# Kernel tuning notes

Hardware: AMD Instinct MI355X
Metric: run time of the kernel (lower is better)

The kernel has to match this reference:

```python
import jax, jax.numpy as jnp
import numpy as np

D = 256          # d_model
NH = 8           # n_heads
HD = D // NH
LEV = 3          # n_levels
NP = 4           # n_points
DFF = 1024       # d_ffn
B = 8            # batch
LQ = 3600        # 60*60 queries (hardcoded in get_reference_points)
SHAPES = np.array([[60, 60], [30, 30], [15, 15]], dtype=np.int64)
LIN = int((SHAPES[:, 0] * SHAPES[:, 1]).sum())  # 4725
START = np.concatenate([[0], np.cumsum(SHAPES[:, 0] * SHAPES[:, 1])[:-1]]).astype(np.int64)


def setup_inputs() -> dict:
    key = jax.random.key(0)
    ks = iter(jax.random.split(key, 32))
    def lin(k, o, i):
        return jax.random.normal(k, (o, i), jnp.float32) * 0.02
    return {
        "tgt": jax.random.normal(next(ks), (LQ, B, D), jnp.float32),
        "query_pos": jax.random.normal(next(ks), (1, 1, D), jnp.float32),
        "src": jax.random.normal(next(ks), (B, LIN, D), jnp.float32),
        "src_spatial_shapes": jnp.asarray(SHAPES),
        "level_start_index": jnp.asarray(START),
        "in_proj_w": lin(next(ks), 3 * D, D),
        "in_proj_b": jnp.zeros((3 * D,), jnp.float32),
        "out_proj_w": lin(next(ks), D, D),
        "out_proj_b": jnp.zeros((D,), jnp.float32),
        "samp_off_w": lin(next(ks), NH * LEV * NP * 2, D),
        "samp_off_b": jax.random.normal(next(ks), (NH * LEV * NP * 2,), jnp.float32) * 0.5,
        "attn_w_w": lin(next(ks), NH * LEV * NP, D),
        "attn_w_b": jnp.zeros((NH * LEV * NP,), jnp.float32),
        "value_proj_w": lin(next(ks), D, D),
        "value_proj_b": jnp.zeros((D,), jnp.float32),
        "cross_out_w": lin(next(ks), D, D),
        "cross_out_b": jnp.zeros((D,), jnp.float32),
        "ln1_g": jnp.ones((D,), jnp.float32), "ln1_b": jnp.zeros((D,), jnp.float32),
        "ln2_g": jnp.ones((D,), jnp.float32), "ln2_b": jnp.zeros((D,), jnp.float32),
        "ln3_g": jnp.ones((D,), jnp.float32), "ln3_b": jnp.zeros((D,), jnp.float32),
        "ffn_w1": lin(next(ks), DFF, D), "ffn_b1": jnp.zeros((DFF,), jnp.float32),
        "ffn_w2": lin(next(ks), D, DFF), "ffn_b2": jnp.zeros((D,), jnp.float32),
    }


def _ln(x, g, b, eps=1e-5):
    m = x.mean(-1, keepdims=True)
    v = ((x - m) ** 2).mean(-1, keepdims=True)
    return (x - m) * jax.lax.rsqrt(v + eps) * g + b


def _self_attn(q_in, k_in, v_in, wqkv, bqkv, wo, bo):
    # torch nn.MultiheadAttention semantics, inputs laid out (seq, batch, embed)
    S, N, _ = q_in.shape
    q = (q_in @ wqkv[:D].T + bqkv[:D]).reshape(S, N, NH, HD)
    k = (k_in @ wqkv[D:2 * D].T + bqkv[D:2 * D]).reshape(S, N, NH, HD)
    v = (v_in @ wqkv[2 * D:].T + bqkv[2 * D:]).reshape(S, N, NH, HD)
    logits = jnp.einsum('snhd,tnhd->nhst', q, k) / np.sqrt(HD).astype(np.float32)
    a = jax.nn.softmax(logits, -1)
    ctx = jnp.einsum('nhst,tnhd->snhd', a, v).reshape(S, N, D)
    return ctx @ wo.T + bo


def _bilinear(v_l, loc, Hl, Wl):
    # v_l: [B, NH, Hl*Wl, HD]; loc: [B, NH, LQ, NP, 2] normalized in [0,1]
    # grid_sample(align_corners=False, padding=zeros): pixel = loc*size - 0.5
    x = loc[..., 0] * Wl - 0.5
    y = loc[..., 1] * Hl - 0.5
    x0 = jnp.floor(x); y0 = jnp.floor(y)
    fx = x - x0; fy = y - y0
    x0 = x0.astype(jnp.int32); y0 = y0.astype(jnp.int32)
    def corner(yi, xi, w):
        valid = ((xi >= 0) & (xi < Wl) & (yi >= 0) & (yi < Hl)).astype(v_l.dtype)
        idx = jnp.clip(yi, 0, Hl - 1) * Wl + jnp.clip(xi, 0, Wl - 1)
        b, h, lq, p = idx.shape
        g = jnp.take_along_axis(v_l, idx.reshape(b, h, lq * p)[..., None], axis=2)
        return g.reshape(b, h, lq, p, HD) * (w * valid)[..., None]
    return (corner(y0, x0, (1 - fx) * (1 - fy))
            + corner(y0, x0 + 1, fx * (1 - fy))
            + corner(y0 + 1, x0, (1 - fx) * fy)
            + corner(y0 + 1, x0 + 1, fx * fy))


def _msdeform(query, ref, src, wso, bso, waw, baw, wv, bv, wo, bo):
    Bq, Lq, _ = query.shape
    value = (src @ wv.T + bv).reshape(Bq, LIN, NH, HD).transpose(0, 2, 1, 3)  # [B,NH,LIN,HD]
    off = (query @ wso.T + bso).reshape(Bq, Lq, NH, LEV, NP, 2)
    aw = (query @ waw.T + baw).reshape(Bq, Lq, NH, LEV * NP)
    aw = jax.nn.softmax(aw, -1).reshape(Bq, Lq, NH, LEV, NP)
    normalizer = jnp.asarray(SHAPES[:, ::-1].copy(), jnp.float32)  # (W, H) per level
    loc = ref[:, :, None, :, None, :] + off / normalizer[None, None, None, :, None, :]
    out = jnp.zeros((Bq, NH, Lq, HD), query.dtype)
    for l in range(LEV):
        Hl, Wl = int(SHAPES[l, 0]), int(SHAPES[l, 1])
        s = int(START[l])
        v_l = value[:, :, s:s + Hl * Wl]
        loc_l = loc[:, :, :, l].transpose(0, 2, 1, 3, 4)      # [B,NH,LQ,NP,2]
        sampled = _bilinear(v_l, loc_l, Hl, Wl)               # [B,NH,LQ,NP,HD]
        out = out + (sampled * aw[:, :, :, l].transpose(0, 2, 1, 3)[..., None]).sum(3)
    out = out.transpose(0, 2, 1, 3).reshape(Bq, Lq, D)
    return out @ wo.T + bo


def _reference_points():
    Hh = Ww = 60
    ys = (jnp.arange(Hh, dtype=jnp.float32) + 0.5) / Hh
    xs = (jnp.arange(Ww, dtype=jnp.float32) + 0.5) / Ww
    yy, xx = jnp.meshgrid(ys, xs, indexing='ij')
    ref = jnp.stack([xx.reshape(-1), yy.reshape(-1)], -1)[None]  # [1, 3600, 2]
    return jnp.broadcast_to(ref[:, :, None, :], (1, Hh * Ww, LEV, 2))


def reference(tgt, query_pos, src, src_spatial_shapes, level_start_index,
              in_proj_w, in_proj_b, out_proj_w, out_proj_b,
              samp_off_w, samp_off_b, attn_w_w, attn_w_b,
              value_proj_w, value_proj_b, cross_out_w, cross_out_b,
              ln1_g, ln1_b, ln2_g, ln2_b, ln3_g, ln3_b,
              ffn_w1, ffn_b1, ffn_w2, ffn_b2):
    # dropout layers are identity (eval mode). spatial shapes are static metadata
    # (SHAPES/START) since slicing sizes must be static under jit.
    q = (tgt + query_pos).transpose(1, 0, 2)
    tgt2 = _self_attn(q, q, tgt.transpose(1, 0, 2), in_proj_w, in_proj_b, out_proj_w, out_proj_b)
    t = _ln(tgt + tgt2.transpose(1, 0, 2), ln2_g, ln2_b)
    ref = _reference_points()
    tq = t.transpose(1, 0, 2)  # permute(1,0,2) -> [B, LQ, D]
    tgt2 = _msdeform(tq + query_pos, ref, src, samp_off_w, samp_off_b,
                     attn_w_w, attn_w_b, value_proj_w, value_proj_b,
                     cross_out_w, cross_out_b)
    tq = _ln(tq + tgt2, ln1_g, ln1_b)
    ff = jax.nn.relu(tq @ ffn_w1.T + ffn_b1) @ ffn_w2.T + ffn_b2
    tq = _ln(tq + ff, ln3_g, ln3_b)
    return tq.transpose(1, 0, 2)  # [LQ, B, D]
```

## Files before the change

### kernel.cpp

```cpp
#include <hip/hip_runtime.h>
#include <hip/hip_bf16.h>
#include <cstddef>
#include <cstdint>

#define D_MODEL 256
#define NHEAD   8
#define HDIM    32
#define NLEV    3
#define NPNT    4
#define DFF     1024
#define BATCH   8
#define LQ      3600
#define LIN     4725
#define MROWS   (BATCH*LQ)

typedef short bf16x8 __attribute__((ext_vector_type(8)));
typedef float f32x4  __attribute__((ext_vector_type(4)));

__device__ __forceinline__ unsigned short f2b(float x) {
    unsigned int u = __float_as_uint(x);
    unsigned int r = (u + 0x7fffu + ((u >> 16) & 1u)) >> 16;
    return (unsigned short)r;
}
__device__ __forceinline__ float b2f(unsigned short s) {
    return __uint_as_float(((unsigned int)s) << 16);
}

#define GLDS16(g, l) __builtin_amdgcn_global_load_lds( \
    (const __attribute__((address_space(1))) void*)(g), \
    (__attribute__((address_space(3))) void*)(l), 16, 0, 0)

#define WAIT_VM0()  asm volatile("s_waitcnt vmcnt(0)" ::: "memory")
#define WAIT_LGKM0() asm volatile("s_waitcnt lgkmcnt(0)" ::: "memory")

#define WTOT 991232
__global__ __launch_bounds__(256) void prep_kernel(
    const float* __restrict__ tgt, unsigned short* __restrict__ tgtb,
    const float* __restrict__ srcf, unsigned short* __restrict__ srcb,
    const float* __restrict__ w_in, const float* __restrict__ w_out,
    const float* __restrict__ w_val, const float* __restrict__ w_cross,
    const float* __restrict__ w_so, const float* __restrict__ w_aw,
    const float* __restrict__ w_f1, const float* __restrict__ w_f2,
    unsigned short* __restrict__ wdst,
    const float* __restrict__ qp, const float* __restrict__ so_b,
    const float* __restrict__ aw_b, float* __restrict__ qpv)
{
    const int bid = blockIdx.x;
    const int tid = threadIdx.x;
    if (bid < 7200) {
        int i = bid * 256 + tid;
        float4 v = ((const float4*)tgt)[i];
        ushort4 o; o.x = f2b(v.x); o.y = f2b(v.y); o.z = f2b(v.z); o.w = f2b(v.w);
        ((ushort4*)tgtb)[i] = o;
    } else if (bid < 16650) {
        int i = (bid - 7200) * 256 + tid;
        float4 v = ((const float4*)srcf)[i];
        ushort4 o; o.x = f2b(v.x); o.y = f2b(v.y); o.z = f2b(v.z); o.w = f2b(v.w);
        ((ushort4*)srcb)[i] = o;
    } else if (bid < 17618) {
        int idx = ((bid - 16650) * 256 + tid) * 4;
        if (idx >= WTOT) return;
        const float* src; int off;
        if      (idx < 196608) { src = w_in;    off = idx; }
        else if (idx < 262144) { src = w_out;   off = idx - 196608; }
        else if (idx < 327680) { src = w_val;   off = idx - 262144; }
        else if (idx < 393216) { src = w_cross; off = idx - 327680; }
        else if (idx < 442368) { src = w_so;    off = idx - 393216; }
        else if (idx < 466944) { src = w_aw;    off = idx - 442368; }
        else if (idx < 729088) { src = w_f1;    off = idx - 466944; }
        else                   { src = w_f2;    off = idx - 729088; }
        float4 v = *(const float4*)(src + off);
        ushort4 o; o.x = f2b(v.x); o.y = f2b(v.y); o.z = f2b(v.z); o.w = f2b(v.w);
        *(ushort4*)(wdst + idx) = o;
    } else {
        int o = (bid - 17618) * 256 + tid;
        if (o >= 768 + 192 + 96) return;
        const float* wrow;
        if (o < 768)       wrow = w_in + (size_t)o * D_MODEL;
        else if (o < 960)  wrow = w_so + (size_t)(o - 768) * D_MODEL;
        else               wrow = w_aw + (size_t)(o - 960) * D_MODEL;
        float acc = 0.f;
        for (int d = 0; d < D_MODEL; ++d) acc += qp[d] * wrow[d];
        qpv[o] = acc;
        if (o >= 768) {
            float bias = (o < 960) ? so_b[o - 768] : aw_b[o - 960];
            qpv[1056 + (o - 768)] = acc + bias;
        }
    }
}

__global__ __launch_bounds__(256) void gemm_bf16(
    const unsigned short* __restrict__ A,
    const unsigned short* __restrict__ W,
    const float* __restrict__ bias,
    const float* __restrict__ bias2, int b2lim,
    float* __restrict__ Cf, unsigned short* __restrict__ Cb,
    int M, int N, int K, int relu)
{
    __shared__ __align__(16) unsigned short As[2 * 128 * 32];
    __shared__ __align__(16) unsigned short Bs[2 * 128 * 32];
    const int tid  = threadIdx.x;
    const int wave = tid >> 6;
    const int lane = tid & 63;
    const int m0 = blockIdx.x * 128;
    const int n0 = blockIdx.y * 128;

    const int lr  = lane >> 2;
    const int lc8 = (lane & 3) * 8;
    int ar0 = m0 + wave * 32 + lr;      if (ar0 > M - 1) ar0 = M - 1;
    int ar1 = m0 + wave * 32 + 16 + lr; if (ar1 > M - 1) ar1 = M - 1;
    int br0 = n0 + wave * 32 + lr;      if (br0 > N - 1) br0 = N - 1;
    int br1 = n0 + wave * 32 + 16 + lr; if (br1 > N - 1) br1 = N - 1;
    const unsigned short* pa0 = A + (size_t)ar0 * K + lc8;
    const unsigned short* pa1 = A + (size_t)ar1 * K + lc8;
    const unsigned short* pb0 = W + (size_t)br0 * K + lc8;
    const unsigned short* pb1 = W + (size_t)br1 * K + lc8;
    unsigned short* la0 = As + wave * 1024;
    unsigned short* la1 = As + wave * 1024 + 512;
    unsigned short* lb0 = Bs + wave * 1024;
    unsigned short* lb1 = Bs + wave * 1024 + 512;

    const int wm = (wave >> 1) * 64;
    const int wn = (wave & 1) * 64;
    const int fr = lane & 15;
    const int fk = (lane >> 4) * 8;

    f32x4 acc[4][4] = {};

    for (int k0 = 0; k0 < K; k0 += 64) {
        GLDS16(pa0, la0); GLDS16(pa0 + 32, la0 + 4096);
        GLDS16(pa1, la1); GLDS16(pa1 + 32, la1 + 4096);
        GLDS16(pb0, lb0); GLDS16(pb0 + 32, lb0 + 4096);
        GLDS16(pb1, lb1); GLDS16(pb1 + 32, lb1 + 4096);
        pa0 += 64; pa1 += 64; pb0 += 64; pb1 += 64;
        __syncthreads();
#pragma unroll
        for (int p = 0; p < 2; ++p) {
            bf16x8 af[4], bfv[4];
#pragma unroll
            for (int i = 0; i < 4; ++i)
                af[i] = *(const bf16x8*)&As[p * 4096 + (wm + i * 16 + fr) * 32 + fk];
#pragma unroll
            for (int j = 0; j < 4; ++j)
                bfv[j] = *(const bf16x8*)&Bs[p * 4096 + (wn + j * 16 + fr) * 32 + fk];
#pragma unroll
            for (int i = 0; i < 4; ++i)
#pragma unroll
                for (int j = 0; j < 4; ++j)
                    acc[i][j] = __builtin_amdgcn_mfma_f32_16x16x32_bf16(
                        af[i], bfv[j], acc[i][j], 0, 0, 0);
        }
        __syncthreads();
    }

    const int quad = lane >> 4;
#pragma unroll
    for (int j = 0; j < 4; ++j) {
        const int col = n0 + wn + j * 16 + fr;
        if (col >= N) continue;
        float bv = 0.f;
        if (bias) bv += bias[col];
        if (bias2 && col < b2lim) bv += bias2[col];
#pragma unroll
        for (int i = 0; i < 4; ++i) {
#pragma unroll
            for (int r = 0; r < 4; ++r) {
                const int row = m0 + wm + i * 16 + quad * 4 + r;
                if (row >= M) continue;
                float v = acc[i][j][r] + bv;
                if (relu) v = fmaxf(v, 0.f);
                if (Cf) Cf[(size_t)row * N + col] = v;
                if (Cb) Cb[(size_t)row * N + col] = f2b(v);
            }
        }
    }
}

__global__ __launch_bounds__(256) void gemm_ln(
    const unsigned short* __restrict__ A,
    const unsigned short* __restrict__ W,
    const float* __restrict__ bias,
    const float* __restrict__ resid,
    const float* __restrict__ g, const float* __restrict__ bb,
    float* __restrict__ outf, unsigned short* __restrict__ outb, int K)
{
    __shared__ __align__(16) unsigned short As[2 * 64 * 32];
    __shared__ __align__(16) unsigned short Bs[2 * 256 * 32];
    const int tid  = threadIdx.x;
    const int wave = tid >> 6;
    const int lane = tid & 63;
    const int m0 = blockIdx.x * 64;

    const int arow = tid >> 2;
    const int akc  = (tid & 3) * 8;
    const unsigned short* pa = A + (size_t)(m0 + arow) * K + akc;
    unsigned short* la = As + tid * 8;
    const unsigned short* pb0 = W + (size_t)(arow)       * K + akc;
    const unsigned short* pb1 = W + (size_t)(64  + arow) * K + akc;
    const unsigned short* pb2 = W + (size_t)(128 + arow) * K + akc;
    const unsigned short* pb3 = W + (size_t)(192 + arow) * K + akc;
    unsigned short* lb0 = Bs + tid * 8;
    unsigned short* lb1 = Bs + 2048 + tid * 8;
    unsigned short* lb2 = Bs + 4096 + tid * 8;
    unsigned short* lb3 = Bs + 6144 + tid * 8;

    const int fr = lane & 15;
    const int fk = (lane >> 4) * 8;
    const int quad = lane >> 4;
    const int colbase = wave * 64;

    f32x4 acc[4][4] = {};

    for (int k0 = 0; k0 < K; k0 += 64) {
        GLDS16(pa, la);        GLDS16(pa + 32, la + 2048);
        GLDS16(pb0, lb0);      GLDS16(pb0 + 32, lb0 + 8192);
        GLDS16(pb1, lb1);      GLDS16(pb1 + 32, lb1 + 8192);
        GLDS16(pb2, lb2);      GLDS16(pb2 + 32, lb2 + 8192);
        GLDS16(pb3, lb3);      GLDS16(pb3 + 32, lb3 + 8192);
        pa += 64; pb0 += 64; pb1 += 64; pb2 += 64; pb3 += 64;
        __syncthreads();
#pragma unroll
        for (int p = 0; p < 2; ++p) {
            bf16x8 af[4], bfv[4];
#pragma unroll
            for (int i = 0; i < 4; ++i)
                af[i] = *(const bf16x8*)&As[p * 2048 + (i * 16 + fr) * 32 + fk];
#pragma unroll
            for (int j = 0; j < 4; ++j)
                bfv[j] = *(const bf16x8*)&Bs[p * 8192 + (colbase + j * 16 + fr) * 32 + fk];
#pragma unroll
            for (int i = 0; i < 4; ++i)
#pragma unroll
                for (int j = 0; j < 4; ++j)
                    acc[i][j] = __builtin_amdgcn_mfma_f32_16x16x32_bf16(
                        af[i], bfv[j], acc[i][j], 0, 0, 0);
        }
        __syncthreads();
    }

    float2* red = (float2*)As;
    float rs[4][4], rq[4][4];
#pragma unroll
    for (int i = 0; i < 4; ++i) {
#pragma unroll
        for (int r = 0; r < 4; ++r) {
            const int row = m0 + i * 16 + quad * 4 + r;
            float s = 0.f, q = 0.f;
#pragma unroll
            for (int j = 0; j < 4; ++j) {
                const int col = colbase + j * 16 + fr;
                float v = acc[i][j][r] + bias[col] + resid[(size_t)row * 256 + col];
                acc[i][j][r] = v;
                s += v; q += v * v;
            }
            rs[i][r] = s; rq[i][r] = q;
        }
    }
#pragma unroll
    for (int off = 1; off < 16; off <<= 1) {
#pragma unroll
        for (int i = 0; i < 4; ++i)
#pragma unroll
            for (int r = 0; r < 4; ++r) {
                rs[i][r] += __shfl_xor(rs[i][r], off);
                rq[i][r] += __shfl_xor(rq[i][r], off);
            }
    }
    if ((lane & 15) == 0) {
#pragma unroll
        for (int i = 0; i < 4; ++i)
#pragma unroll
            for (int r = 0; r < 4; ++r)
                red[wave * 64 + i * 16 + quad * 4 + r] = make_float2(rs[i][r], rq[i][r]);
    }
    __syncthreads();
#pragma unroll
    for (int i = 0; i < 4; ++i) {
#pragma unroll
        for (int r = 0; r < 4; ++r) {
            const int rl = i * 16 + quad * 4 + r;
            const float2 t0 = red[rl], t1 = red[64 + rl], t2 = red[128 + rl], t3 = red[192 + rl];
            const float sum = t0.x + t1.x + t2.x + t3.x;
            const float sq  = t0.y + t1.y + t2.y + t3.y;
            const float mean = sum * (1.f / 256.f);
            const float var  = sq * (1.f / 256.f) - mean * mean;
            const float inv  = rsqrtf(var + 1e-5f);
            const int row = m0 + rl;
#pragma unroll
            for (int j = 0; j < 4; ++j) {
                const int col = colbase + j * 16 + fr;
                const float val = (acc[i][j][r] - mean) * inv * g[col] + bb[col];
                outf[(size_t)row * 256 + col] = val;
                if (outb) outb[(size_t)row * 256 + col] = f2b(val);
            }
        }
    }
}

__global__ __launch_bounds__(256) void cross_ffn_kernel(
    const unsigned short* __restrict__ A,
    const unsigned short* __restrict__ Wcr,
    const float* __restrict__ bcr,
    const float* __restrict__ resid1,
    const float* __restrict__ g1, const float* __restrict__ b1g,
    float* __restrict__ t2,
    const unsigned short* __restrict__ W1,
    const float* __restrict__ b1,
    const unsigned short* __restrict__ W2,
    const float* __restrict__ b2,
    const float* __restrict__ g3, const float* __restrict__ b3g,
    float* __restrict__ outf)
{
    __shared__ __align__(16) unsigned short Wc[16384];
    __shared__ __align__(16) unsigned short hid[2304];
    const int tid  = threadIdx.x;
    const int wave = tid >> 6;
    const int lane = tid & 63;
    const int m0 = blockIdx.x * 32;
    const int fr   = lane & 15;
    const int quad = lane >> 4;
    const int xm   = fr & 7;
    float2* red = (float2*)hid;

#pragma unroll
    for (int j = 0; j < 4; ++j) {
        const int c  = wave * 4 + j;
        const int rA = c * 2 + (lane >> 5);
        const int k8 = (lane & 31) ^ (rA & 7);
        GLDS16(A + (size_t)(m0 + rA) * 256 + k8 * 8, Wc + c * 512);
    }
    int w1off[8], w2off[8];
#pragma unroll
    for (int j = 0; j < 8; ++j) {
        const int c  = wave * 8 + j;
        const int n1 = c * 2 + (lane >> 5);
        const int k1 = (lane & 31) ^ (n1 & 7);
        w1off[j] = n1 * 256 + k1 * 8;
        const int n2 = c * 8 + (lane >> 3);
        const int k2 = (lane & 7) ^ (n2 & 7);
        w2off[j] = n2 * 1024 + k2 * 8;
    }
    __syncthreads();
    bf16x8 af[2][8];
#pragma unroll
    for (int i = 0; i < 2; ++i)
#pragma unroll
        for (int s = 0; s < 8; ++s)
            af[i][s] = *(const bf16x8*)&Wc[((i * 16 + fr) * 32 + ((s * 4 + quad) ^ xm)) * 8];
    WAIT_LGKM0();
    __syncthreads();

#pragma unroll
    for (int j = 0; j < 8; ++j)
        GLDS16(Wcr + w1off[j], Wc + (wave * 8 + j) * 512);
    f32x4 accc[4][2] = {};
    for (int c = 0; c < 4; ++c) {
        WAIT_VM0();
        bf16x8 bv[8];
#pragma unroll
        for (int s = 0; s < 8; ++s)
            bv[s] = *(const bf16x8*)&Wc[((wave * 16 + fr) * 32 + ((s * 4 + quad) ^ xm)) * 8];
        WAIT_LGKM0();
        if (c < 3) {
#pragma unroll
            for (int j = 0; j < 8; ++j)
                GLDS16(Wcr + (size_t)(c + 1) * 16384 + w1off[j], Wc + (wave * 8 + j) * 512);
        }
#pragma unroll
        for (int s = 0; s < 8; ++s) {
            accc[c][0] = __builtin_amdgcn_mfma_f32_16x16x32_bf16(af[0][s], bv[s], accc[c][0], 0, 0, 0);
            accc[c][1] = __builtin_amdgcn_mfma_f32_16x16x32_bf16(af[1][s], bv[s], accc[c][1], 0, 0, 0);
        }
    }

    float rs[2][4], rq[2][4];
#pragma unroll
    for (int x = 0; x < 2; ++x) {
#pragma unroll
        for (int r = 0; r < 4; ++r) {
            const int row = m0 + x * 16 + quad * 4 + r;
            float s = 0.f, q = 0.f;
#pragma unroll
            for (int c = 0; c < 4; ++c) {
                const int col = c * 64 + wave * 16 + fr;
                float v = accc[c][x][r] + bcr[col] + resid1[(size_t)row * 256 + col];
                accc[c][x][r] = v;
                s += v; q += v * v;
            }
            rs[x][r] = s; rq[x][r] = q;
        }
    }
#pragma unroll
    for (int off = 1; off < 16; off <<= 1) {
#pragma unroll
        for (int x = 0; x < 2; ++x)
#pragma unroll
            for (int r = 0; r < 4; ++r) {
                rs[x][r] += __shfl_xor(rs[x][r], off);
                rq[x][r] += __shfl_xor(rq[x][r], off);
            }
    }
    if ((lane & 15) == 0) {
#pragma unroll
        for (int x = 0; x < 2; ++x)
#pragma unroll
            for (int r = 0; r < 4; ++r)
                red[wave * 32 + x * 16 + quad * 4 + r] = make_float2(rs[x][r], rq[x][r]);
    }
    __syncthreads();
#pragma unroll
    for (int x = 0; x < 2; ++x) {
#pragma unroll
        for (int r = 0; r < 4; ++r) {
            const int rl = x * 16 + quad * 4 + r;
            const float2 t0 = red[rl], t1 = red[32 + rl], t2r = red[64 + rl], t3 = red[96 + rl];
            const float sum = t0.x + t1.x + t2r.x + t3.x;
            const float sq  = t0.y + t1.y + t2r.y + t3.y;
            const float mean = sum * (1.f / 256.f);
            const float var  = sq * (1.f / 256.f) - mean * mean;
            const float inv  = rsqrtf(var + 1e-5f);
            const int row = m0 + rl;
#pragma unroll
            for (int c = 0; c < 4; ++c) {
                const int col = c * 64 + wave * 16 + fr;
                const float val = (accc[c][x][r] - mean) * inv * g1[col] + b1g[col];
                t2[(size_t)row * 256 + col] = val;
                const int g8 = col >> 3;
                Wc[rl * 256 + ((g8 ^ (rl & 7)) << 3) + (col & 7)] = f2b(val);
            }
        }
    }
    __syncthreads();
#pragma unroll
    for (int i = 0; i < 2; ++i)
#pragma unroll
        for (int s = 0; s < 8; ++s)
            af[i][s] = *(const bf16x8*)&Wc[((i * 16 + fr) * 32 + ((s * 4 + quad) ^ xm)) * 8];
    WAIT_LGKM0();
    __syncthreads();

#pragma unroll
    for (int j = 0; j < 8; ++j)
        GLDS16(W1 + w1off[j], Wc + (wave * 8 + j) * 512);
    WAIT_VM0();

    f32x4 acc2[2][4] = {};

    for (int h = 0; h < 16; ++h) {
        bf16x8 bv[8];
#pragma unroll
        for (int s = 0; s < 8; ++s)
            bv[s] = *(const bf16x8*)&Wc[((wave * 16 + fr) * 32 + ((s * 4 + quad) ^ xm)) * 8];
        WAIT_LGKM0();
#pragma unroll
        for (int j = 0; j < 8; ++j)
            GLDS16(W2 + (size_t)h * 64 + w2off[j], Wc + (wave * 8 + j) * 512);
        f32x4 acc1[2] = {};
#pragma unroll
        for (int s = 0; s < 8; ++s) {
            acc1[0] = __builtin_amdgcn_mfma_f32_16x16x32_bf16(af[0][s], bv[s], acc1[0], 0, 0, 0);
            acc1[1] = __builtin_amdgcn_mfma_f32_16x16x32_bf16(af[1][s], bv[s], acc1[1], 0, 0, 0);
        }
        const float bias1 = b1[h * 64 + wave * 16 + fr];
#pragma unroll
        for (int i = 0; i < 2; ++i)
#pragma unroll
            for (int r = 0; r < 4; ++r) {
                float v = fmaxf(acc1[i][r] + bias1, 0.f);
                hid[(i * 16 + quad * 4 + r) * 72 + wave * 16 + fr] = f2b(v);
            }
        __syncthreads();
#pragma unroll
        for (int s = 0; s < 2; ++s) {
            bf16x8 a2[2], b2v[4];
#pragma unroll
            for (int j2 = 0; j2 < 4; ++j2) {
                const int nb = wave * 64 + j2 * 16 + fr;
                b2v[j2] = *(const bf16x8*)&Wc[(nb * 8 + ((s * 4 + quad) ^ xm)) * 8];
            }
#pragma unroll
            for (int i = 0; i < 2; ++i)
                a2[i] = *(const bf16x8*)&hid[(i * 16 + fr) * 72 + s * 32 + quad * 8];
            if (s == 1) {
                WAIT_LGKM0();
                if (h < 15) {
#pragma unroll
                    for (int j = 0; j < 8; ++j)
                        GLDS16(W1 + (size_t)(h + 1) * 16384 + w1off[j], Wc + (wave * 8 + j) * 512);
                }
            }
#pragma unroll
            for (int i = 0; i < 2; ++i)
#pragma unroll
                for (int j2 = 0; j2 < 4; ++j2)
                    acc2[i][j2] = __builtin_amdgcn_mfma_f32_16x16x32_bf16(
                        a2[i], b2v[j2], acc2[i][j2], 0, 0, 0);
        }
        __syncthreads();
    }

    const int colbase = wave * 64;
#pragma unroll
    for (int x = 0; x < 2; ++x) {
#pragma unroll
        for (int r = 0; r < 4; ++r) {
            const int row = m0 + x * 16 + quad * 4 + r;
            float s = 0.f, q = 0.f;
#pragma unroll
            for (int y = 0; y < 4; ++y) {
                const int col = colbase + y * 16 + fr;
                float v = acc2[x][y][r] + b2[col] + t2[(size_t)row * 256 + col];
                acc2[x][y][r] = v;
                s += v; q += v * v;
            }
            rs[x][r] = s; rq[x][r] = q;
        }
    }
#pragma unroll
    for (int off = 1; off < 16; off <<= 1) {
#pragma unroll
        for (int x = 0; x < 2; ++x)
#pragma unroll
            for (int r = 0; r < 4; ++r) {
                rs[x][r] += __shfl_xor(rs[x][r], off);
                rq[x][r] += __shfl_xor(rq[x][r], off);
            }
    }
    if ((lane & 15) == 0) {
#pragma unroll
        for (int x = 0; x < 2; ++x)
#pragma unroll
            for (int r = 0; r < 4; ++r)
                red[wave * 32 + x * 16 + quad * 4 + r] = make_float2(rs[x][r], rq[x][r]);
    }
    __syncthreads();
#pragma unroll
    for (int x = 0; x < 2; ++x) {
#pragma unroll
        for (int r = 0; r < 4; ++r) {
            const int rl = x * 16 + quad * 4 + r;
            const float2 t0 = red[rl], t1 = red[32 + rl], t2r = red[64 + rl], t3 = red[96 + rl];
            const float sum = t0.x + t1.x + t2r.x + t3.x;
            const float sq  = t0.y + t1.y + t2r.y + t3.y;
            const float mean = sum * (1.f / 256.f);
            const float var  = sq * (1.f / 256.f) - mean * mean;
            const float inv  = rsqrtf(var + 1e-5f);
            const int row = m0 + rl;
#pragma unroll
            for (int y = 0; y < 4; ++y) {
                const int col = colbase + y * 16 + fr;
                outf[(size_t)row * 256 + col] = (acc2[x][y][r] - mean) * inv * g3[col] + b3g[col];
            }
        }
    }
}

__global__ __launch_bounds__(256) void self_attn_kernel(
    const unsigned short* __restrict__ qkv, unsigned short* __restrict__ ctx)
{
    __shared__ float sh[8][768];
    __shared__ float ls[8][8][8];
    __shared__ __align__(16) unsigned short ob[2048];
    const int n = blockIdx.x;
    const int t = threadIdx.x;

    const unsigned short* base = qkv + (size_t)n * 8 * 768;
#pragma unroll
    for (int i = 0; i < 3; ++i) {
        const int idx = (i * 256 + t) * 8;
        bf16x8 v = *(const bf16x8*)&base[idx];
        const int s = idx / 768;
        const int c = idx - s * 768;
#pragma unroll
        for (int j = 0; j < 8; ++j)
            sh[s][c + j] = b2f((unsigned short)v[j]);
    }
    __syncthreads();
    const int h = t >> 5, j = t & 31;
#pragma unroll
    for (int pair = j; pair < 64; pair += 32) {
        const int s = pair >> 3, tt = pair & 7;
        float acc = 0.f;
#pragma unroll
        for (int d = 0; d < 32; ++d)
            acc += sh[s][h * 32 + d] * sh[tt][256 + h * 32 + d];
        ls[h][s][tt] = acc * 0.17677669529663687f;
    }
    __syncthreads();
    if (t < 64) {
        const int hh = t >> 3, s = t & 7;
        float mx = -1e30f;
        for (int tt = 0; tt < 8; ++tt) mx = fmaxf(mx, ls[hh][s][tt]);
        float sum = 0.f;
        for (int tt = 0; tt < 8; ++tt) { float e = expf(ls[hh][s][tt] - mx); ls[hh][s][tt] = e; sum += e; }
        const float inv = 1.f / sum;
        for (int tt = 0; tt < 8; ++tt) ls[hh][s][tt] *= inv;
    }
    __syncthreads();
#pragma unroll
    for (int s = 0; s < 8; ++s) {
        float acc = 0.f;
#pragma unroll
        for (int tt = 0; tt < 8; ++tt)
            acc += ls[h][s][tt] * sh[tt][512 + h * 32 + j];
        ob[s * 256 + t] = f2b(acc);
    }
    __syncthreads();
    ((bf16x8*)ctx)[(size_t)n * 256 + t] = ((const bf16x8*)ob)[t];
}

__global__ __launch_bounds__(256) void msdeform_kernel(
    const unsigned short* __restrict__ value,
    const float* __restrict__ comb,
    unsigned short* __restrict__ out)
{
    const int bid = blockIdx.x;
    const int b   = bid & 7;
    const int lq0 = (bid >> 3) * 4;
    const int r    = threadIdx.x >> 6;
    const int lane = threadIdx.x & 63;
    const int h = lane >> 3;
    const int l = lane & 7;
    const int lq = lq0 + r;
    const int m = lq * 8 + b;

    const float* offp = comb + (size_t)m * 288 + h * 24;
    const float* awp  = comb + (size_t)m * 288 + 192 + h * 12;
    float off[24], aw[12];
#pragma unroll
    for (int i = 0; i < 6; ++i) *(float4*)&off[i * 4] = ((const float4*)offp)[i];
#pragma unroll
    for (int i = 0; i < 3; ++i) *(float4*)&aw[i * 4] = ((const float4*)awp)[i];

    float mx = aw[0];
#pragma unroll
    for (int i = 1; i < 12; ++i) mx = fmaxf(mx, aw[i]);
    float se = 0.f;
#pragma unroll
    for (int i = 0; i < 12; ++i) { aw[i] = __expf(aw[i] - mx); se += aw[i]; }
    const float inv = 1.f / se;

    const float refx = ((lq % 60) + 0.5f) * (1.f / 60.f);
    const float refy = ((lq / 60) + 0.5f) * (1.f / 60.f);
    const int HW[3] = {60, 30, 15};
    const int ST[3] = {0, 3600, 4500};

    const unsigned short* vbase = value + (size_t)b * LIN * 256 + h * 32 + l * 4;

    float a0 = 0.f, a1 = 0.f, a2 = 0.f, a3 = 0.f;
#pragma unroll
    for (int lev = 0; lev < NLEV; ++lev) {
        const int Wl = HW[lev], s0 = ST[lev];
        const float fWl = (float)Wl;
#pragma unroll
        for (int p = 0; p < NPNT; ++p) {
            const int pt = lev * 4 + p;
            const float ox = off[lev * 8 + p * 2];
            const float oy = off[lev * 8 + p * 2 + 1];
            const float px = refx * fWl + ox - 0.5f;
            const float py = refy * fWl + oy - 0.5f;
            const float x0f = floorf(px), y0f = floorf(py);
            const float fx = px - x0f, fy = py - y0f;
            const int x0 = (int)x0f, y0 = (int)y0f;
            const float aww = aw[pt] * inv;
            const float vx0 = (x0 >= 0 && x0 < Wl) ? 1.f : 0.f;
            const float vx1 = (x0 >= -1 && x0 < Wl - 1) ? 1.f : 0.f;
            const float vy0 = (y0 >= 0 && y0 < Wl) ? 1.f : 0.f;
            const float vy1 = (y0 >= -1 && y0 < Wl - 1) ? 1.f : 0.f;
            const int xc0 = min(max(x0, 0), Wl - 1);
            const int xc1 = min(max(x0 + 1, 0), Wl - 1);
            const int yc0 = min(max(y0, 0), Wl - 1);
            const int yc1 = min(max(y0 + 1, 0), Wl - 1);
            const int sx  = xc1 - xc0;
            const int syW = (yc1 - yc0) * Wl;
            const int i00 = s0 + yc0 * Wl + xc0;
            const float w00 = (1.f - fx) * (1.f - fy) * aww * vx0 * vy0;
            const float w01 = fx * (1.f - fy) * aww * vx1 * vy0;
            const float w10 = (1.f - fx) * fy * aww * vx0 * vy1;
            const float w11 = fx * fy * aww * vx1 * vy1;
            const int i01 = i00 + sx;
            const int i10 = i00 + syW;
            const int i11 = i10 + sx;
            const ushort4 g00 = *(const ushort4*)(vbase + (size_t)i00 * 256);
            const ushort4 g01 = *(const ushort4*)(vbase + (size_t)i01 * 256);
            const ushort4 g10 = *(const ushort4*)(vbase + (size_t)i10 * 256);
            const ushort4 g11 = *(const ushort4*)(vbase + (size_t)i11 * 256);
            a0 += b2f(g00.x) * w00 + b2f(g01.x) * w01 + b2f(g10.x) * w10 + b2f(g11.x) * w11;
            a1 += b2f(g00.y) * w00 + b2f(g01.y) * w01 + b2f(g10.y) * w10 + b2f(g11.y) * w11;
            a2 += b2f(g00.z) * w00 + b2f(g01.z) * w01 + b2f(g10.z) * w10 + b2f(g11.z) * w11;
            a3 += b2f(g00.w) * w00 + b2f(g01.w) * w01 + b2f(g10.w) * w10 + b2f(g11.w) * w11;
        }
    }
    ushort4 o;
    o.x = f2b(a0); o.y = f2b(a1); o.z = f2b(a2); o.w = f2b(a3);
    *(ushort4*)(out + (size_t)m * 256 + h * 32 + l * 4) = o;
}

extern "C" void kernel_launch(void* const* d_in, const int* in_sizes, int n_in,
                              void* d_out, int out_size, void* d_ws, size_t ws_size,
                              hipStream_t stream)
{
    (void)in_sizes; (void)n_in; (void)out_size; (void)ws_size;
    const float* tgt          = (const float*)d_in[0];
    const float* qp           = (const float*)d_in[1];
    const float* src          = (const float*)d_in[2];
    const float* in_proj_w    = (const float*)d_in[5];
    const float* in_proj_b    = (const float*)d_in[6];
    const float* out_proj_w   = (const float*)d_in[7];
    const float* out_proj_b   = (const float*)d_in[8];
    const float* samp_off_w   = (const float*)d_in[9];
    const float* samp_off_b   = (const float*)d_in[10];
    const float* attn_w_w     = (const float*)d_in[11];
    const float* attn_w_b     = (const float*)d_in[12];
    const float* value_proj_w = (const float*)d_in[13];
    const float* value_proj_b = (const float*)d_in[14];
    const float* cross_out_w  = (const float*)d_in[15];
    const float* cross_out_b  = (const float*)d_in[16];
    const float* ln1_g = (const float*)d_in[17];
    const float* ln1_b = (const float*)d_in[18];
    const float* ln2_g = (const float*)d_in[19];
    const float* ln2_b = (const float*)d_in[20];
    const float* ln3_g = (const float*)d_in[21];
    const float* ln3_b = (const float*)d_in[22];
    const float* ffn_w1 = (const float*)d_in[23];
    const float* ffn_b1 = (const float*)d_in[24];
    const float* ffn_w2 = (const float*)d_in[25];
    const float* ffn_b2 = (const float*)d_in[26];
    float* out = (float*)d_out;

    float* ws    = (float*)d_ws;
    float* t     = ws;
    float* t2    = ws + 7372800;
    float* comb  = ws + 14745600;
    float* qpv   = ws + 23040000;
    float* cbias = qpv + 1056;

    unsigned short* bws    = (unsigned short*)((char*)d_ws + 92165376);
    unsigned short* s1     = bws;
    unsigned short* tgtb   = s1;
    unsigned short* ctxb   = s1;
    unsigned short* tb     = s1;
    unsigned short* s2     = bws + 7372800;
    unsigned short* qkvb   = s2;
    unsigned short* valueb = s2;
    unsigned short* msoutb = s2 + 9676800;
    unsigned short* srcb   = bws + 36864000;
    unsigned short* wtsb   = bws + 46540800;

    prep_kernel<<<17623, 256, 0, stream>>>(tgt, tgtb, src, srcb,
                                           in_proj_w, out_proj_w, value_proj_w,
                                           cross_out_w, samp_off_w, attn_w_w,
                                           ffn_w1, ffn_w2, wtsb,
                                           qp, samp_off_b, attn_w_b, qpv);
    gemm_bf16<<<dim3(225, 6), 256, 0, stream>>>(tgtb, wtsb + 0, in_proj_b, qpv, 512,
                                                nullptr, qkvb, MROWS, 768, 256, 0);
    self_attn_kernel<<<3600, 256, 0, stream>>>(qkvb, ctxb);
    gemm_ln<<<450, 256, 0, stream>>>(ctxb, wtsb + 196608, out_proj_b, tgt,
                                     ln2_g, ln2_b, t, tb, 256);
    gemm_bf16<<<dim3(296, 2), 256, 0, stream>>>(srcb, wtsb + 262144, value_proj_b, nullptr, 0,
                                                nullptr, valueb, BATCH * LIN, 256, 256, 0);
    gemm_bf16<<<dim3(225, 3), 256, 0, stream>>>(tb, wtsb + 393216, cbias, nullptr, 0,
                                                comb, nullptr, MROWS, 288, 256, 0);
    msdeform_kernel<<<7200, 256, 0, stream>>>(valueb, comb, msoutb);
    cross_ffn_kernel<<<900, 256, 0, stream>>>(msoutb, wtsb + 327680, cross_out_b,
                                              t, ln1_g, ln1_b, t2,
                                              wtsb + 466944, ffn_b1,
                                              wtsb + 729088, ffn_b2,
                                              ln3_g, ln3_b, out);
}
```

Measured before the change: 445.6 us.

## Fuse out-proj+LN2 with sampling-offset/attn-weight GEMM in one kernel

Replaces the out-projection+LayerNorm kernel and the following offsets/attention-weight GEMM with a single kernel. Each block handles 32 rows, keeps the normalized bf16 rows in shared memory, and streams both weight matrices through a swizzled LDS buffer in 64-column chunks. This removes the bf16 intermediate round trip through global memory and one kernel launch. In exchange, smaller row tiles mean weights are re-read by more blocks, and the chunk loop stalls on a full memory-wait each step.

```diff
diff --git a/kernel.cpp b/kernel.cpp
--- a/kernel.cpp
+++ b/kernel.cpp
@@ -176,124 +176,185 @@
     }
 }
 
-__global__ __launch_bounds__(256) void gemm_ln(
+__global__ __launch_bounds__(256) void ln2_offs_kernel(
     const unsigned short* __restrict__ A,
-    const unsigned short* __restrict__ W,
-    const float* __restrict__ bias,
+    const unsigned short* __restrict__ Wo,
+    const float* __restrict__ bo,
     const float* __restrict__ resid,
-    const float* __restrict__ g, const float* __restrict__ bb,
-    float* __restrict__ outf, unsigned short* __restrict__ outb, int K)
+    const float* __restrict__ g2, const float* __restrict__ b2g,
+    float* __restrict__ tout,
+    const unsigned short* __restrict__ Wso,
+    const float* __restrict__ cbias,
+    float* __restrict__ comb)
 {
-    __shared__ __align__(16) unsigned short As[2 * 64 * 32];
-    __shared__ __align__(16) unsigned short Bs[2 * 256 * 32];
+    __shared__ __align__(16) unsigned short Wc[16384];
+    __shared__ float2 red[128];
     const int tid  = threadIdx.x;
     const int wave = tid >> 6;
     const int lane = tid & 63;
-    const int m0 = blockIdx.x * 64;
-
-    const int arow = tid >> 2;
-    const int akc  = (tid & 3) * 8;
-    const unsigned short* pa = A + (size_t)(m0 + arow) * K + akc;
-    unsigned short* la = As + tid * 8;
-    const unsigned short* pb0 = W + (size_t)(arow)       * K + akc;
-    const unsigned short* pb1 = W + (size_t)(64  + arow) * K + akc;
-    const unsigned short* pb2 = W + (size_t)(128 + arow) * K + akc;
-    const unsigned short* pb3 = W + (size_t)(192 + arow) * K + akc;
-    unsigned short* lb0 = Bs + tid * 8;
-    unsigned short* lb1 = Bs + 2048 + tid * 8;
-    unsigned short* lb2 = Bs + 4096 + tid * 8;
-    unsigned short* lb3 = Bs + 6144 + tid * 8;
-
-    const int fr = lane & 15;
-    const int fk = (lane >> 4) * 8;
+    const int m0 = blockIdx.x * 32;
+    const int fr   = lane & 15;
     const int quad = lane >> 4;
-    const int colbase = wave * 64;
-
-    f32x4 acc[4][4] = {};
-
-    for (int k0 = 0; k0 < K; k0 += 64) {
-        GLDS16(pa, la);        GLDS16(pa + 32, la + 2048);
-        GLDS16(pb0, lb0);      GLDS16(pb0 + 32, lb0 + 8192);
-        GLDS16(pb1, lb1);      GLDS16(pb1 + 32, lb1 + 8192);
-        GLDS16(pb2, lb2);      GLDS16(pb2 + 32, lb2 + 8192);
-        GLDS16(pb3, lb3);      GLDS16(pb3 + 32, lb3 + 8192);
-        pa += 64; pb0 += 64; pb1 += 64; pb2 += 64; pb3 += 64;
-        __syncthreads();
-#pragma unroll
-        for (int p = 0; p < 2; ++p) {
-            bf16x8 af[4], bfv[4];
-#pragma unroll
-            for (int i = 0; i < 4; ++i)
-                af[i] = *(const bf16x8*)&As[p * 2048 + (i * 16 + fr) * 32 + fk];
-#pragma unroll
-            for (int j = 0; j < 4; ++j)
-                bfv[j] = *(const bf16x8*)&Bs[p * 8192 + (colbase + j * 16 + fr) * 32 + fk];
-#pragma unroll
-            for (int i = 0; i < 4; ++i)
-#pragma unroll
-                for (int j = 0; j < 4; ++j)
-                    acc[i][j] = __builtin_amdgcn_mfma_f32_16x16x32_bf16(
-                        af[i], bfv[j], acc[i][j], 0, 0, 0);
-        }
-        __syncthreads();
-    }
-
-    float2* red = (float2*)As;
-    float rs[4][4], rq[4][4];
-#pragma unroll
-    for (int i = 0; i < 4; ++i) {
+    const int xm   = fr & 7;
+
+#pragma unroll
+    for (int j = 0; j < 4; ++j) {
+        const int c  = wave * 4 + j;
+        const int rA = c * 2 + (lane >> 5);
+        const int k8 = (lane & 31) ^ (rA & 7);
+        GLDS16(A + (size_t)(m0 + rA) * 256 + k8 * 8, Wc + c * 512);
+    }
+    int w1off[8], w4off[8];
+#pragma unroll
+    for (int j = 0; j < 8; ++j) {
+        const int c  = wave * 8 + j;
+        const int n1 = c * 2 + (lane >> 5);
+        const int k1 = (lane & 31) ^ (n1 & 7);
+        w1off[j] = n1 * 256 + k1 * 8;
+        const int n4 = (n1 < 32) ? n1 : 31;
+        const int k4 = (lane & 31) ^ (n4 & 7);
+        w4off[j] = n4 * 256 + k4 * 8;
+    }
+    __syncthreads();
+    bf16x8 af[2][8];
+#pragma unroll
+    for (int i = 0; i < 2; ++i)
+#pragma unroll
+        for (int s = 0; s < 8; ++s)
+            af[i][s] = *(const bf16x8*)&Wc[((i * 16 + fr) * 32 + ((s * 4 + quad) ^ xm)) * 8];
+    WAIT_LGKM0();
+    __syncthreads();
+
+#pragma unroll
+    for (int j = 0; j < 8; ++j)
+        GLDS16(Wo + w1off[j], Wc + (wave * 8 + j) * 512);
+    f32x4 accc[4][2] = {};
+    for (int c = 0; c < 4; ++c) {
+        WAIT_VM0();
+        bf16x8 bv[8];
+#pragma unroll
+        for (int s = 0; s < 8; ++s)
+            bv[s] = *(const bf16x8*)&Wc[((wave * 16 + fr) * 32 + ((s * 4 + quad) ^ xm)) * 8];
+        WAIT_LGKM0();
+        if (c < 3) {
+#pragma unroll
+            for (int j = 0; j < 8; ++j)
+                GLDS16(Wo + (size_t)(c + 1) * 16384 + w1off[j], Wc + (wave * 8 + j) * 512);
+        }
+#pragma unroll
+        for (int s = 0; s < 8; ++s) {
+            accc[c][0] = __builtin_amdgcn_mfma_f32_16x16x32_bf16(af[0][s], bv[s], accc[c][0], 0, 0, 0);
+            accc[c][1] = __builtin_amdgcn_mfma_f32_16x16x32_bf16(af[1][s], bv[s], accc[c][1], 0, 0, 0);
+        }
+    }
+
+    float rs[2][4], rq[2][4];
+#pragma unroll
+    for (int x = 0; x < 2; ++x) {
 #pragma unroll
         for (int r = 0; r < 4; ++r) {
-            const int row = m0 + i * 16 + quad * 4 + r;
+            const int row = m0 + x * 16 + quad * 4 + r;
             float s = 0.f, q = 0.f;
 #pragma unroll
-            for (int j = 0; j < 4; ++j) {
-                const int col = colbase + j * 16 + fr;
-                float v = acc[i][j][r] + bias[col] + resid[(size_t)row * 256 + col];
-                acc[i][j][r] = v;
+            for (int c = 0; c < 4; ++c) {
+                const int col = c * 64 + wave * 16 + fr;
+                float v = accc[c][x][r] + bo[col] + resid[(size_t)row * 256 + col];
+                accc[c][x][r] = v;
                 s += v; q += v * v;
             }
-            rs[i][r] = s; rq[i][r] = q;
+            rs[x][r] = s; rq[x][r] = q;
         }
     }
 #pragma unroll
     for (int off = 1; off < 16; off <<= 1) {
 #pragma unroll
-        for (int i = 0; i < 4; ++i)
+        for (int x = 0; x < 2; ++x)
 #pragma unroll
             for (int r = 0; r < 4; ++r) {
-                rs[i][r] += __shfl_xor(rs[i][r], off);
-                rq[i][r] += __shfl_xor(rq[i][r], off);
+                rs[x][r] += __shfl_xor(rs[x][r], off);
+                rq[x][r] += __shfl_xor(rq[x][r], off);
             }
     }
     if ((lane & 15) == 0) {
 #pragma unroll
-        for (int i = 0; i < 4; ++i)
+        for (int x = 0; x < 2; ++x)
 #pragma unroll
             for (int r = 0; r < 4; ++r)
-                red[wave * 64 + i * 16 + quad * 4 + r] = make_float2(rs[i][r], rq[i][r]);
-    }
-    __syncthreads();
-#pragma unroll
-    for (int i = 0; i < 4; ++i) {
+                red[wave * 32 + x * 16 + quad * 4 + r] = make_float2(rs[x][r], rq[x][r]);
+    }
+    __syncthreads();
+#pragma unroll
+    for (int x = 0; x < 2; ++x) {
 #pragma unroll
         for (int r = 0; r < 4; ++r) {
-            const int rl = i * 16 + quad * 4 + r;
-            const float2 t0 = red[rl], t1 = red[64 + rl], t2 = red[128 + rl], t3 = red[192 + rl];
-            const float sum = t0.x + t1.x + t2.x + t3.x;
-            const float sq  = t0.y + t1.y + t2.y + t3.y;
+            const int rl = x * 16 + quad * 4 + r;
+            const float2 t0 = red[rl], t1 = red[32 + rl], t2r = red[64 + rl], t3 = red[96 + rl];
+            const float sum = t0.x + t1.x + t2r.x + t3.x;
+            const float sq  = t0.y + t1.y + t2r.y + t3.y;
             const float mean = sum * (1.f / 256.f);
             const float var  = sq * (1.f / 256.f) - mean * mean;
             const float inv  = rsqrtf(var + 1e-5f);
             const int row = m0 + rl;
 #pragma unroll
-            for (int j = 0; j < 4; ++j) {
-                const int col = colbase + j * 16 + fr;
-                const float val = (acc[i][j][r] - mean) * inv * g[col] + bb[col];
-                outf[(size_t)row * 256 + col] = val;
-                if (outb) outb[(size_t)row * 256 + col] = f2b(val);
-            }
-        }
+            for (int c = 0; c < 4; ++c) {
+                const int col = c * 64 + wave * 16 + fr;
+                const float val = (accc[c][x][r] - mean) * inv * g2[col] + b2g[col];
+                tout[(size_t)row * 256 + col] = val;
+                const int g8 = col >> 3;
+                Wc[rl * 256 + ((g8 ^ (rl & 7)) << 3) + (col & 7)] = f2b(val);
+            }
+        }
+    }
+    __syncthreads();
+#pragma unroll
+    for (int i = 0; i < 2; ++i)
+#pragma unroll
+        for (int s = 0; s < 8; ++s)
+            af[i][s] = *(const bf16x8*)&Wc[((i * 16 + fr) * 32 + ((s * 4 + quad) ^ xm)) * 8];
+    WAIT_LGKM0();
+    __syncthreads();
+
+#pragma unroll
+    for (int j = 0; j < 8; ++j)
+        GLDS16(Wso + w1off[j], Wc + (wave * 8 + j) * 512);
+    f32x4 accP[5][2] = {};
+    for (int c = 0; c < 5; ++c) {
+        WAIT_VM0();
+        bf16x8 bv[8];
+#pragma unroll
+        for (int s = 0; s < 8; ++s)
+            bv[s] = *(const bf16x8*)&Wc[((wave * 16 + fr) * 32 + ((s * 4 + quad) ^ xm)) * 8];
+        WAIT_LGKM0();
+        if (c < 4) {
+            if (c < 3) {
+#pragma unroll
+                for (int j = 0; j < 8; ++j)
+                    GLDS16(Wso + (size_t)(c + 1) * 16384 + w1off[j], Wc + (wave * 8 + j) * 512);
+            } else {
+#pragma unroll
+                for (int j = 0; j < 8; ++j)
+                    GLDS16(Wso + (size_t)4 * 16384 + w4off[j], Wc + (wave * 8 + j) * 512);
+            }
+        }
+#pragma unroll
+        for (int s = 0; s < 8; ++s) {
+            accP[c][0] = __builtin_amdgcn_mfma_f32_16x16x32_bf16(af[0][s], bv[s], accP[c][0], 0, 0, 0);
+            accP[c][1] = __builtin_amdgcn_mfma_f32_16x16x32_bf16(af[1][s], bv[s], accP[c][1], 0, 0, 0);
+        }
+    }
+
+#pragma unroll
+    for (int c = 0; c < 5; ++c) {
+        const int col = c * 64 + wave * 16 + fr;
+        if (col >= 288) continue;
+        const float cb = cbias[col];
+#pragma unroll
+        for (int x = 0; x < 2; ++x)
+#pragma unroll
+            for (int r = 0; r < 4; ++r) {
+                const int row = m0 + x * 16 + quad * 4 + r;
+                comb[(size_t)row * 288 + col] = accP[c][x][r] + cb;
+            }
     }
 }
 
@@ -739,7 +800,6 @@
     unsigned short* s1     = bws;
     unsigned short* tgtb   = s1;
     unsigned short* ctxb   = s1;
-    unsigned short* tb     = s1;
     unsigned short* s2     = bws + 7372800;
     unsigned short* qkvb   = s2;
     unsigned short* valueb = s2;
@@ -755,12 +815,11 @@
     gemm_bf16<<<dim3(225, 6), 256, 0, stream>>>(tgtb, wtsb + 0, in_proj_b, qpv, 512,
                                                 nullptr, qkvb, MROWS, 768, 256, 0);
     self_attn_kernel<<<3600, 256, 0, stream>>>(qkvb, ctxb);
-    gemm_ln<<<450, 256, 0, stream>>>(ctxb, wtsb + 196608, out_proj_b, tgt,
-                                     ln2_g, ln2_b, t, tb, 256);
+    ln2_offs_kernel<<<900, 256, 0, stream>>>(ctxb, wtsb + 196608, out_proj_b,
+                                             tgt, ln2_g, ln2_b, t,
+                                             wtsb + 393216, cbias, comb);
     gemm_bf16<<<dim3(296, 2), 256, 0, stream>>>(srcb, wtsb + 262144, value_proj_b, nullptr, 0,
                                                 nullptr, valueb, BATCH * LIN, 256, 256, 0);
-    gemm_bf16<<<dim3(225, 3), 256, 0, stream>>>(tb, wtsb + 393216, cbias, nullptr, 0,
-                                                comb, nullptr, MROWS, 288, 256, 0);
     msdeform_kernel<<<7200, 256, 0, stream>>>(valueb, comb, msoutb);
     cross_ffn_kernel<<<900, 256, 0, stream>>>(msoutb, wtsb + 327680, cross_out_b,
                                               t, ln1_g, ln1_b, t2,
```

New measurement: 444.5 us. About the same (-0.2%).
